# Kernel optimization log

Measured on AMD Instinct MI355X. Metric: run time of the kernel, lower is better.

The kernel has to match this reference:

```python
import jax, jax.numpy as jnp
import numpy as np

N, D, H, E = 50000, 512, 8, 3200000
DK = D // H  # 64


def setup_inputs() -> dict:
    key = jax.random.key(0)
    ks = jax.random.split(key, 12)
    x = jax.random.normal(ks[0], (N, D), dtype=jnp.float32)
    row_index = jnp.sort(jax.random.randint(ks[1], (E,), 0, N))
    col_index = jax.random.randint(ks[2], (E,), 0, N)
    att_bias = jax.random.normal(ks[3], (H, E), dtype=jnp.float32)
    # xavier-uniform-ish linear params (bias zero per module init)
    lim = np.sqrt(6.0 / (D + D)).astype(np.float32)
    def w(k):
        return jax.random.uniform(k, (D, D), minval=-lim, maxval=lim, dtype=jnp.float32)
    return {
        "x": x, "row_index": row_index, "col_index": col_index, "att_bias": att_bias,
        "Wq": w(ks[4]), "bq": jnp.zeros((D,), jnp.float32),
        "Wk": w(ks[5]), "bk": jnp.zeros((D,), jnp.float32),
        "Wv": w(ks[6]), "bv": jnp.zeros((D,), jnp.float32),
        "Wo": w(ks[7]), "bo": jnp.zeros((D,), jnp.float32),
    }


def _proj(x, W, b):
    # nn.Linear then reshape(N, H, DK).permute(1,0,2) -> [H, N, DK]
    return (x @ W.T + b).reshape(x.shape[0], H, DK).transpose(1, 0, 2)


def reference(x, row_index, col_index, att_bias, Wq, bq, Wk, bk, Wv, bv, Wo, bo):
    q = _proj(x, Wq, bq) / jnp.sqrt(jnp.float32(DK))  # [H,N,DK]
    k = _proj(x, Wk, bk)
    v = _proj(x, Wv, bv)
    n = x.shape[0]
    # masked QK^T at sparse (row,col) entries + additive sparse bias -> [H,E]
    logits = jnp.einsum("hed,hed->he", q[:, row_index], k[:, col_index]) + att_bias
    # per-row (segment) softmax over CSR rows, vmapped over heads
    seg_max = jax.vmap(lambda l: jax.ops.segment_max(l, row_index, num_segments=n))(logits)  # [H,N]
    p = jnp.exp(logits - seg_max[:, row_index])
    denom = jax.vmap(lambda pe: jax.ops.segment_sum(pe, row_index, num_segments=n))(p)  # [H,N]
    att = p / denom[:, row_index]  # [H,E]
    # sparse att @ V : scatter-add weighted value rows
    y = jax.vmap(lambda a, vc: jax.ops.segment_sum(a[:, None] * vc, row_index, num_segments=n))(
        att, v[:, col_index]
    )  # [H,N,DK]
    y = y.transpose(1, 0, 2).reshape(n, H * DK)  # [N,D]
    return y @ Wo.T + bo
```

## Files before the change

kernel.cpp:

```cpp
#include <hip/hip_runtime.h>
#include <hip/hip_bf16.h>
#include <cstddef>
#include <cstdint>


typedef __attribute__((ext_vector_type(8))) short bf16x8;
typedef __attribute__((ext_vector_type(4))) float f32x4;

#define KQ_SCALE 25.4f
#define KQ_DEQ   0.03937007874f

__device__ __forceinline__ void gload_lds16(const void* g, const void* l) {
    __builtin_amdgcn_global_load_lds(
        (const __attribute__((address_space(1))) unsigned int*)g,
        (__attribute__((address_space(3))) unsigned int*)l, 16, 0, 0);
}

__device__ __forceinline__ float bflo(unsigned u) { return __uint_as_float(u << 16); }
__device__ __forceinline__ float bfhi(unsigned u) { return __uint_as_float(u & 0xffff0000u); }
__device__ __forceinline__ float ub(unsigned u, int i) {
    return (float)((u >> (i * 8)) & 0xffu);
}

__device__ __forceinline__ void storeT(float* p, size_t i, float v) { p[i] = v; }
__device__ __forceinline__ void storeT(__hip_bfloat16* p, size_t i, float v) {
    p[i] = __float2bfloat16(v);
}
__device__ __forceinline__ void storeT(unsigned char* p, size_t i, float v) {
    const float q = fmaf(v, KQ_SCALE, 128.0f);
    p[i] = (unsigned char)__float2uint_rn(fminf(fmaxf(q, 0.f), 255.f));
}

__global__ __launch_bounds__(256) void conv_f32_bf16(
    const float* __restrict__ s, __hip_bfloat16* __restrict__ d, int n) {
    const int i = (blockIdx.x * 256 + threadIdx.x) * 8;
    if (i >= n) return;
    const float4 a = *(const float4*)(s + i);
    const float4 b = *(const float4*)(s + i + 4);
    alignas(16) __hip_bfloat16 o[8] = {
        __float2bfloat16(a.x), __float2bfloat16(a.y),
        __float2bfloat16(a.z), __float2bfloat16(a.w),
        __float2bfloat16(b.x), __float2bfloat16(b.y),
        __float2bfloat16(b.z), __float2bfloat16(b.w)};
    *(uint4*)(d + i) = *(const uint4*)o;
}

__global__ void row_start_kernel(const int* __restrict__ row_index,
                                 int* __restrict__ row_start, int n_rows, int E) {
    const int n = blockIdx.x * blockDim.x + threadIdx.x;
    if (n > n_rows) return;
    int lo = 0, hi = E;
    while (lo < hi) {
        const int mid = (lo + hi) >> 1;
        if (row_index[mid] < n) lo = mid + 1; else hi = mid;
    }
    row_start[n] = lo;
}

template <typename TO>
__global__ __launch_bounds__(256) void gemm_mfma_kernel(
    const short* __restrict__ A, const short* __restrict__ Bw,
    const float* __restrict__ bias, TO* __restrict__ C, int M, float scale) {
    __shared__ short As[128 * 32];
    __shared__ short Bs[128 * 32];
    const int t = threadIdx.x;
    const int w = t >> 6, l = t & 63;
    const int m0 = blockIdx.x * 128, n0 = blockIdx.y * 128;
    const int wrow = (w >> 1) * 64, wcol = (w & 1) * 64;
    const int fr = l & 15, fq = l >> 4;

    const int r0 = (w * 64 + l) >> 2, ko0 = ((w * 64 + l) & 3) * 8;
    int gmA0 = m0 + r0;      if (gmA0 >= M) gmA0 = M - 1;
    int gmA1 = m0 + r0 + 64; if (gmA1 >= M) gmA1 = M - 1;
    const int gnB0 = n0 + r0, gnB1 = n0 + r0 + 64;

    f32x4 acc[4][4];
#pragma unroll
    for (int mi = 0; mi < 4; ++mi)
#pragma unroll
        for (int ni = 0; ni < 4; ++ni) acc[mi][ni] = (f32x4){0.f, 0.f, 0.f, 0.f};

    for (int k0 = 0; k0 < 512; k0 += 32) {
        __syncthreads();
        gload_lds16(A + (size_t)gmA0 * 512 + k0 + ko0, As + w * 512);
        gload_lds16(A + (size_t)gmA1 * 512 + k0 + ko0, As + 2048 + w * 512);
        gload_lds16(Bw + (size_t)gnB0 * 512 + k0 + ko0, Bs + w * 512);
        gload_lds16(Bw + (size_t)gnB1 * 512 + k0 + ko0, Bs + 2048 + w * 512);
        __syncthreads();

        bf16x8 af[4], bfr[4];
#pragma unroll
        for (int mi = 0; mi < 4; ++mi)
            af[mi] = *(const bf16x8*)(As + (wrow + mi * 16 + fr) * 32 + fq * 8);
#pragma unroll
        for (int ni = 0; ni < 4; ++ni)
            bfr[ni] = *(const bf16x8*)(Bs + (wcol + ni * 16 + fr) * 32 + fq * 8);
#pragma unroll
        for (int mi = 0; mi < 4; ++mi)
#pragma unroll
            for (int ni = 0; ni < 4; ++ni)
                acc[mi][ni] = __builtin_amdgcn_mfma_f32_16x16x32_bf16(
                    af[mi], bfr[ni], acc[mi][ni], 0, 0, 0);
    }

#pragma unroll
    for (int mi = 0; mi < 4; ++mi)
#pragma unroll
        for (int ni = 0; ni < 4; ++ni)
#pragma unroll
            for (int r = 0; r < 4; ++r) {
                const int gr = m0 + wrow + mi * 16 + fq * 4 + r;
                if (gr < M) {
                    const int gc = n0 + wcol + ni * 16 + fr;
                    storeT(C, (size_t)gr * 512 + gc, (acc[mi][ni][r] + bias[gc]) * scale);
                }
            }
}

__global__ __launch_bounds__(256) void sparse_attn_kernel(
    const __hip_bfloat16* __restrict__ qb, const unsigned char* __restrict__ kq,
    const unsigned char* __restrict__ vq, const int* __restrict__ col_index,
    const float* __restrict__ att_bias, const int* __restrict__ row_start,
    __hip_bfloat16* __restrict__ yout, int E) {
    const int n = blockIdx.x;
    const int w = threadIdx.x >> 6;
    const int lane = threadIdx.x & 63;
    const int g = lane & 7;
    const int j = lane >> 3;
    const int hA = 2 * w + (g >> 2);
    const int dim0 = (g & 3) * 16;
    const int e0 = row_start[n], e1 = row_start[n + 1];

    const short* qp = (const short*)qb + (size_t)n * 512 + hA * 64 + dim0;
    float qf[16];
    {
        const uint4 a = *(const uint4*)qp;
        const uint4 b = *(const uint4*)(qp + 8);
        const unsigned* ua = (const unsigned*)&a;
        const unsigned* ubp = (const unsigned*)&b;
#pragma unroll
        for (int i = 0; i < 4; ++i) {
            qf[2 * i]     = bflo(ua[i]);
            qf[2 * i + 1] = bfhi(ua[i]);
            qf[8 + 2 * i]     = bflo(ubp[i]);
            qf[8 + 2 * i + 1] = bfhi(ubp[i]);
        }
    }
    float sumq = 0.f;
#pragma unroll
    for (int i = 0; i < 16; ++i) sumq += qf[i];
    sumq += __shfl_xor(sumq, 1, 64);
    sumq += __shfl_xor(sumq, 2, 64);
    const float qc = -128.0f * KQ_DEQ * sumq;

    const float* biasH = att_bias + (size_t)hA * (size_t)E;
    const unsigned pairoff = (unsigned)(w * 128 + g * 16);

    float acc[16];
#pragma unroll
    for (int i = 0; i < 16; ++i) acc[i] = 0.f;
    float s_lane = 0.f;

    if (e0 < e1) {
        const int e1m1 = e1 - 1;
#pragma unroll 2
        for (int base = e0; base < e1; base += 8) {
            const int e = base + j;
            const int ec = min(e, e1m1);
            const int c = col_index[ec];
            const unsigned co = ((unsigned)c << 9) + pairoff;
            const uint4 ku = *(const uint4*)(kq + co);
            const uint4 vu = *(const uint4*)(vq + co);
            const float bv = biasH[ec];

            float d = 0.f;
            {
                const unsigned* u = (const unsigned*)&ku;
#pragma unroll
                for (int i = 0; i < 4; ++i)
#pragma unroll
                    for (int b = 0; b < 4; ++b)
                        d = fmaf(qf[4 * i + b], ub(u[i], b), d);
            }
            d += __shfl_xor(d, 1, 64);
            d += __shfl_xor(d, 2, 64);
            const float lg = fmaf(KQ_DEQ, d, qc) + bv;
            const float p = (e < e1) ? __expf(lg) : 0.f;
            s_lane += p;

            {
                const unsigned* u = (const unsigned*)&vu;
#pragma unroll
                for (int i = 0; i < 4; ++i)
#pragma unroll
                    for (int b = 0; b < 4; ++b)
                        acc[4 * i + b] = fmaf(p, ub(u[i], b), acc[4 * i + b]);
            }
        }
    }

#pragma unroll
    for (int st = 8; st < 64; st <<= 1) s_lane += __shfl_xor(s_lane, st, 64);
#pragma unroll
    for (int i = 0; i < 16; ++i) {
#pragma unroll
        for (int st = 8; st < 64; st <<= 1) acc[i] += __shfl_xor(acc[i], st, 64);
    }

    float y0 = acc[0], y1 = acc[1];
#pragma unroll
    for (int t = 1; t < 8; ++t) {
        y0 = (j == t) ? acc[2 * t] : y0;
        y1 = (j == t) ? acc[2 * t + 1] : y1;
    }
    const size_t orow = (size_t)n * 512 + hA * 64 + dim0 + 2 * j;
    if (s_lane > 0.f) {
        const float inv = 1.0f / s_lane;
        yout[orow]     = __float2bfloat16(fmaf(KQ_DEQ, y0 * inv, -128.0f * KQ_DEQ));
        yout[orow + 1] = __float2bfloat16(fmaf(KQ_DEQ, y1 * inv, -128.0f * KQ_DEQ));
    } else {
        yout[orow]     = __float2bfloat16(0.f);
        yout[orow + 1] = __float2bfloat16(0.f);
    }
}

extern "C" void kernel_launch(void* const* d_in, const int* in_sizes, int n_in,
                              void* d_out, int out_size, void* d_ws, size_t ws_size,
                              hipStream_t stream) {
    const float* x         = (const float*)d_in[0];
    const int*   row_index = (const int*)d_in[1];
    const int*   col_index = (const int*)d_in[2];
    const float* att_bias  = (const float*)d_in[3];
    const float* Wq = (const float*)d_in[4];
    const float* bq = (const float*)d_in[5];
    const float* Wk = (const float*)d_in[6];
    const float* bk = (const float*)d_in[7];
    const float* Wv = (const float*)d_in[8];
    const float* bv = (const float*)d_in[9];
    const float* Wo = (const float*)d_in[10];
    const float* bo = (const float*)d_in[11];
    float* out = (float*)d_out;

    const int N = in_sizes[0] / 512;
    const int E = in_sizes[1];
    const int WN = 512 * 512;

    char* ws = (char*)d_ws;
    const size_t nb = (size_t)N * 512 * sizeof(__hip_bfloat16);
    const size_t qb8 = (size_t)N * 512;
    const size_t wb = (size_t)WN * sizeof(__hip_bfloat16);
    __hip_bfloat16* xb  = (__hip_bfloat16*)(ws);
    __hip_bfloat16* qb  = (__hip_bfloat16*)(ws + nb);
    unsigned char*  kqv = (unsigned char*)(ws + 2 * nb);
    unsigned char*  vqv = (unsigned char*)(ws + 2 * nb + qb8);
    __hip_bfloat16* wqb = (__hip_bfloat16*)(ws + 2 * nb + 2 * qb8);
    __hip_bfloat16* wkb = (__hip_bfloat16*)(ws + 2 * nb + 2 * qb8 + wb);
    __hip_bfloat16* wvb = (__hip_bfloat16*)(ws + 2 * nb + 2 * qb8 + 2 * wb);
    __hip_bfloat16* wob = (__hip_bfloat16*)(ws + 2 * nb + 2 * qb8 + 3 * wb);
    int* row_start = (int*)(ws + 2 * nb + 2 * qb8 + 4 * wb);

    conv_f32_bf16<<<(N * 512 / 8 + 255) / 256, 256, 0, stream>>>(x, xb, N * 512);
    conv_f32_bf16<<<(WN / 8 + 255) / 256, 256, 0, stream>>>(Wq, wqb, WN);
    conv_f32_bf16<<<(WN / 8 + 255) / 256, 256, 0, stream>>>(Wk, wkb, WN);
    conv_f32_bf16<<<(WN / 8 + 255) / 256, 256, 0, stream>>>(Wv, wvb, WN);
    conv_f32_bf16<<<(WN / 8 + 255) / 256, 256, 0, stream>>>(Wo, wob, WN);

    row_start_kernel<<<(N + 1 + 255) / 256, 256, 0, stream>>>(row_index, row_start, N, E);

    const dim3 gg((N + 127) / 128, 4), gb(256);
    gemm_mfma_kernel<__hip_bfloat16><<<gg, gb, 0, stream>>>(
        (const short*)xb, (const short*)wqb, bq, qb, N, 0.125f);
    gemm_mfma_kernel<unsigned char><<<gg, gb, 0, stream>>>(
        (const short*)xb, (const short*)wkb, bk, kqv, N, 1.0f);
    gemm_mfma_kernel<unsigned char><<<gg, gb, 0, stream>>>(
        (const short*)xb, (const short*)wvb, bv, vqv, N, 1.0f);

    sparse_attn_kernel<<<N, 256, 0, stream>>>(
        qb, kqv, vqv, col_index, att_bias, row_start, xb , E);

    gemm_mfma_kernel<float><<<gg, gb, 0, stream>>>(
        (const short*)xb, (const short*)wob, bo, out, N, 1.0f);
}
```

Measured before the change: 778.9 us.

## Double-buffer GEMM LDS tiles and software-pipeline sparse attention gathers

The GEMM kernel now uses two LDS buffers, issuing the global-to-LDS loads for the next K tile before computing on the current one, with one barrier per iteration instead of two. The sparse attention loop prefetches the next edge's column index, K/V bytes and bias into registers while it computes the current edge, and the bias is read with nontemporal loads. Both changes aim to hide global memory latency behind compute. The cost is double the GEMM LDS footprint and higher register pressure in the attention kernel, which may reduce occupancy. Workspace pointer names are also renamed.

New measurement: 834.3 us. 7.1% more time.

```diff
diff --git a/kernel.cpp b/kernel.cpp
--- a/kernel.cpp
+++ b/kernel.cpp
@@ -61,8 +61,8 @@
 __global__ __launch_bounds__(256) void gemm_mfma_kernel(
     const short* __restrict__ A, const short* __restrict__ Bw,
     const float* __restrict__ bias, TO* __restrict__ C, int M, float scale) {
-    __shared__ short As[128 * 32];
-    __shared__ short Bs[128 * 32];
+    __shared__ short As[2][128 * 32];
+    __shared__ short Bs[2][128 * 32];
     const int t = threadIdx.x;
     const int w = t >> 6, l = t & 63;
     const int m0 = blockIdx.x * 128, n0 = blockIdx.y * 128;
@@ -80,28 +80,38 @@
 #pragma unroll
         for (int ni = 0; ni < 4; ++ni) acc[mi][ni] = (f32x4){0.f, 0.f, 0.f, 0.f};
 
-    for (int k0 = 0; k0 < 512; k0 += 32) {
-        __syncthreads();
-        gload_lds16(A + (size_t)gmA0 * 512 + k0 + ko0, As + w * 512);
-        gload_lds16(A + (size_t)gmA1 * 512 + k0 + ko0, As + 2048 + w * 512);
-        gload_lds16(Bw + (size_t)gnB0 * 512 + k0 + ko0, Bs + w * 512);
-        gload_lds16(Bw + (size_t)gnB1 * 512 + k0 + ko0, Bs + 2048 + w * 512);
-        __syncthreads();
+#define STAGE(buf, k0)                                                        \
+    do {                                                                      \
+        gload_lds16(A + (size_t)gmA0 * 512 + (k0) + ko0, &As[buf][w * 512]);  \
+        gload_lds16(A + (size_t)gmA1 * 512 + (k0) + ko0, &As[buf][2048 + w * 512]); \
+        gload_lds16(Bw + (size_t)gnB0 * 512 + (k0) + ko0, &Bs[buf][w * 512]); \
+        gload_lds16(Bw + (size_t)gnB1 * 512 + (k0) + ko0, &Bs[buf][2048 + w * 512]); \
+    } while (0)
+
+    STAGE(0, 0);
+    __syncthreads();
+
+    for (int kt = 0; kt < 16; ++kt) {
+        const int cur = kt & 1;
+        if (kt + 1 < 16) STAGE(cur ^ 1, (kt + 1) * 32);
 
         bf16x8 af[4], bfr[4];
 #pragma unroll
         for (int mi = 0; mi < 4; ++mi)
-            af[mi] = *(const bf16x8*)(As + (wrow + mi * 16 + fr) * 32 + fq * 8);
+            af[mi] = *(const bf16x8*)(&As[cur][(wrow + mi * 16 + fr) * 32 + fq * 8]);
 #pragma unroll
         for (int ni = 0; ni < 4; ++ni)
-            bfr[ni] = *(const bf16x8*)(Bs + (wcol + ni * 16 + fr) * 32 + fq * 8);
+            bfr[ni] = *(const bf16x8*)(&Bs[cur][(wcol + ni * 16 + fr) * 32 + fq * 8]);
 #pragma unroll
         for (int mi = 0; mi < 4; ++mi)
 #pragma unroll
             for (int ni = 0; ni < 4; ++ni)
                 acc[mi][ni] = __builtin_amdgcn_mfma_f32_16x16x32_bf16(
                     af[mi], bfr[ni], acc[mi][ni], 0, 0, 0);
-    }
+
+        __syncthreads();
+    }
+#undef STAGE
 
 #pragma unroll
     for (int mi = 0; mi < 4; ++mi)
@@ -163,15 +173,24 @@
 
     if (e0 < e1) {
         const int e1m1 = e1 - 1;
-#pragma unroll 2
+        int ec = min(e0 + j, e1m1);
+        unsigned co = ((unsigned)col_index[ec] << 9) + pairoff;
+        uint4 ku = *(const uint4*)(kq + co);
+        uint4 vu = *(const uint4*)(vq + co);
+        float bv = __builtin_nontemporal_load(biasH + ec);
+        bool vld = (e0 + j) < e1;
+
         for (int base = e0; base < e1; base += 8) {
-            const int e = base + j;
-            const int ec = min(e, e1m1);
-            const int c = col_index[ec];
-            const unsigned co = ((unsigned)c << 9) + pairoff;
-            const uint4 ku = *(const uint4*)(kq + co);
-            const uint4 vu = *(const uint4*)(vq + co);
-            const float bv = biasH[ec];
+            uint4 ku_n, vu_n; float bv_n = 0.f; bool vld_n = false;
+            const int nbase = base + 8;
+            if (nbase < e1) {
+                const int ecn = min(nbase + j, e1m1);
+                const unsigned con = ((unsigned)col_index[ecn] << 9) + pairoff;
+                ku_n = *(const uint4*)(kq + con);
+                vu_n = *(const uint4*)(vq + con);
+                bv_n = __builtin_nontemporal_load(biasH + ecn);
+                vld_n = (nbase + j) < e1;
+            }
 
             float d = 0.f;
             {
@@ -185,9 +204,8 @@
             d += __shfl_xor(d, 1, 64);
             d += __shfl_xor(d, 2, 64);
             const float lg = fmaf(KQ_DEQ, d, qc) + bv;
-            const float p = (e < e1) ? __expf(lg) : 0.f;
+            const float p = vld ? __expf(lg) : 0.f;
             s_lane += p;
-
             {
                 const unsigned* u = (const unsigned*)&vu;
 #pragma unroll
@@ -196,6 +214,8 @@
                     for (int b = 0; b < 4; ++b)
                         acc[4 * i + b] = fmaf(p, ub(u[i], b), acc[4 * i + b]);
             }
+
+            ku = ku_n; vu = vu_n; bv = bv_n; vld = vld_n;
         }
     }
 
@@ -247,17 +267,17 @@
 
     char* ws = (char*)d_ws;
     const size_t nb = (size_t)N * 512 * sizeof(__hip_bfloat16);
-    const size_t qb8 = (size_t)N * 512;
+    const size_t b8 = (size_t)N * 512;
     const size_t wb = (size_t)WN * sizeof(__hip_bfloat16);
     __hip_bfloat16* xb  = (__hip_bfloat16*)(ws);
     __hip_bfloat16* qb  = (__hip_bfloat16*)(ws + nb);
-    unsigned char*  kqv = (unsigned char*)(ws + 2 * nb);
-    unsigned char*  vqv = (unsigned char*)(ws + 2 * nb + qb8);
-    __hip_bfloat16* wqb = (__hip_bfloat16*)(ws + 2 * nb + 2 * qb8);
-    __hip_bfloat16* wkb = (__hip_bfloat16*)(ws + 2 * nb + 2 * qb8 + wb);
-    __hip_bfloat16* wvb = (__hip_bfloat16*)(ws + 2 * nb + 2 * qb8 + 2 * wb);
-    __hip_bfloat16* wob = (__hip_bfloat16*)(ws + 2 * nb + 2 * qb8 + 3 * wb);
-    int* row_start = (int*)(ws + 2 * nb + 2 * qb8 + 4 * wb);
+    unsigned char*  kq8 = (unsigned char*)(ws + 2 * nb);
+    unsigned char*  vq8 = (unsigned char*)(ws + 2 * nb + b8);
+    __hip_bfloat16* wqb = (__hip_bfloat16*)(ws + 2 * nb + 2 * b8);
+    __hip_bfloat16* wkb = (__hip_bfloat16*)(ws + 2 * nb + 2 * b8 + wb);
+    __hip_bfloat16* wvb = (__hip_bfloat16*)(ws + 2 * nb + 2 * b8 + 2 * wb);
+    __hip_bfloat16* wob = (__hip_bfloat16*)(ws + 2 * nb + 2 * b8 + 3 * wb);
+    int* row_start = (int*)(ws + 2 * nb + 2 * b8 + 4 * wb);
 
     conv_f32_bf16<<<(N * 512 / 8 + 255) / 256, 256, 0, stream>>>(x, xb, N * 512);
     conv_f32_bf16<<<(WN / 8 + 255) / 256, 256, 0, stream>>>(Wq, wqb, WN);
@@ -271,12 +291,12 @@
     gemm_mfma_kernel<__hip_bfloat16><<<gg, gb, 0, stream>>>(
         (const short*)xb, (const short*)wqb, bq, qb, N, 0.125f);
     gemm_mfma_kernel<unsigned char><<<gg, gb, 0, stream>>>(
-        (const short*)xb, (const short*)wkb, bk, kqv, N, 1.0f);
+        (const short*)xb, (const short*)wkb, bk, kq8, N, 1.0f);
     gemm_mfma_kernel<unsigned char><<<gg, gb, 0, stream>>>(
-        (const short*)xb, (const short*)wvb, bv, vqv, N, 1.0f);
+        (const short*)xb, (const short*)wvb, bv, vq8, N, 1.0f);
 
     sparse_attn_kernel<<<N, 256, 0, stream>>>(
-        qb, kqv, vqv, col_index, att_bias, row_start, xb , E);
+        qb, kq8, vq8, col_index, att_bias, row_start, xb , E);
 
     gemm_mfma_kernel<float><<<gg, gb, 0, stream>>>(
         (const short*)xb, (const short*)wob, bo, out, N, 1.0f);
```

## Quantize Q to int8 per head and use sdot4 for QK dot products

Applied to the files above, without the earlier changes.

Adds a per-(node,head) int8 quantization of Q and stores K as signed int8, so the sparse attention kernel computes QK logits with integer dot4 instructions instead of unpacking bytes into float FMAs. The attention loop is also unrolled manually to process two edge groups per iteration, interleaving their loads and accumulation. This cuts ALU work and register pressure in the logit stage but adds an extra quantization kernel pass over Q and further loss of precision in the logits.

Result: slower. 831.4 us (+6.7%).

```diff
diff --git a/kernel.cpp b/kernel.cpp
--- a/kernel.cpp
+++ b/kernel.cpp
@@ -10,6 +10,20 @@
 #define KQ_SCALE 25.4f
 #define KQ_DEQ   0.03937007874f
 
+#if __has_builtin(__builtin_amdgcn_sdot4)
+__device__ __forceinline__ int SDOT4(int a, int b, int c) {
+    return __builtin_amdgcn_sdot4(a, b, c, false);
+}
+#else
+__device__ __forceinline__ int SDOT4(int a, int b, int c) {
+#pragma unroll
+    for (int i = 0; i < 4; ++i)
+        c += (int)(signed char)((unsigned)a >> (8 * i)) *
+             (int)(signed char)((unsigned)b >> (8 * i));
+    return c;
+}
+#endif
+
 __device__ __forceinline__ void gload_lds16(const void* g, const void* l) {
     __builtin_amdgcn_global_load_lds(
         (const __attribute__((address_space(1))) unsigned int*)g,
@@ -29,6 +43,9 @@
 __device__ __forceinline__ void storeT(unsigned char* p, size_t i, float v) {
     const float q = fmaf(v, KQ_SCALE, 128.0f);
     p[i] = (unsigned char)__float2uint_rn(fminf(fmaxf(q, 0.f), 255.f));
+}
+__device__ __forceinline__ void storeT(signed char* p, size_t i, float v) {
+    p[i] = (signed char)__float2int_rn(fminf(fmaxf(v, -127.f), 127.f));
 }
 
 __global__ __launch_bounds__(256) void conv_f32_bf16(
@@ -57,6 +74,22 @@
     row_start[n] = lo;
 }
 
+__global__ __launch_bounds__(256) void quant_q_kernel(
+    const __hip_bfloat16* __restrict__ qb, signed char* __restrict__ qi8,
+    float* __restrict__ qdeq, int NH) {
+    const int wid = blockIdx.x * 4 + (threadIdx.x >> 6);
+    if (wid >= NH) return;
+    const int lane = threadIdx.x & 63;
+    const size_t off = (size_t)wid * 64 + lane;
+    const float v = __bfloat162float(qb[off]);
+    float a = fabsf(v);
+#pragma unroll
+    for (int st = 1; st < 64; st <<= 1) a = fmaxf(a, __shfl_xor(a, st, 64));
+    const float scale = (a > 0.f) ? 127.0f / a : 0.f;
+    qi8[off] = (signed char)__float2int_rn(v * scale);
+    if (lane == 0) qdeq[wid] = a * (1.0f / 127.0f);
+}
+
 template <typename TO>
 __global__ __launch_bounds__(256) void gemm_mfma_kernel(
     const short* __restrict__ A, const short* __restrict__ Bw,
@@ -118,10 +151,10 @@
 }
 
 __global__ __launch_bounds__(256) void sparse_attn_kernel(
-    const __hip_bfloat16* __restrict__ qb, const unsigned char* __restrict__ kq,
-    const unsigned char* __restrict__ vq, const int* __restrict__ col_index,
-    const float* __restrict__ att_bias, const int* __restrict__ row_start,
-    __hip_bfloat16* __restrict__ yout, int E) {
+    const signed char* __restrict__ qi8, const float* __restrict__ qdeq,
+    const signed char* __restrict__ kq, const unsigned char* __restrict__ vq,
+    const int* __restrict__ col_index, const float* __restrict__ att_bias,
+    const int* __restrict__ row_start, __hip_bfloat16* __restrict__ yout, int E) {
     const int n = blockIdx.x;
     const int w = threadIdx.x >> 6;
     const int lane = threadIdx.x & 63;
@@ -131,27 +164,8 @@
     const int dim0 = (g & 3) * 16;
     const int e0 = row_start[n], e1 = row_start[n + 1];
 
-    const short* qp = (const short*)qb + (size_t)n * 512 + hA * 64 + dim0;
-    float qf[16];
-    {
-        const uint4 a = *(const uint4*)qp;
-        const uint4 b = *(const uint4*)(qp + 8);
-        const unsigned* ua = (const unsigned*)&a;
-        const unsigned* ubp = (const unsigned*)&b;
-#pragma unroll
-        for (int i = 0; i < 4; ++i) {
-            qf[2 * i]     = bflo(ua[i]);
-            qf[2 * i + 1] = bfhi(ua[i]);
-            qf[8 + 2 * i]     = bflo(ubp[i]);
-            qf[8 + 2 * i + 1] = bfhi(ubp[i]);
-        }
-    }
-    float sumq = 0.f;
-#pragma unroll
-    for (int i = 0; i < 16; ++i) sumq += qf[i];
-    sumq += __shfl_xor(sumq, 1, 64);
-    sumq += __shfl_xor(sumq, 2, 64);
-    const float qc = -128.0f * KQ_DEQ * sumq;
+    const int4 qu = *(const int4*)(qi8 + (size_t)n * 512 + hA * 64 + dim0);
+    const float dsc = qdeq[(size_t)n * 8 + hA] * KQ_DEQ;
 
     const float* biasH = att_bias + (size_t)hA * (size_t)E;
     const unsigned pairoff = (unsigned)(w * 128 + g * 16);
@@ -163,38 +177,49 @@
 
     if (e0 < e1) {
         const int e1m1 = e1 - 1;
-#pragma unroll 2
-        for (int base = e0; base < e1; base += 8) {
-            const int e = base + j;
-            const int ec = min(e, e1m1);
-            const int c = col_index[ec];
-            const unsigned co = ((unsigned)c << 9) + pairoff;
-            const uint4 ku = *(const uint4*)(kq + co);
-            const uint4 vu = *(const uint4*)(vq + co);
-            const float bv = biasH[ec];
-
-            float d = 0.f;
+        for (int base = e0; base < e1; base += 16) {
+            const int eA = base + j, eB = base + 8 + j;
+            const int ecA = min(eA, e1m1), ecB = min(eB, e1m1);
+            const int cA = col_index[ecA], cB = col_index[ecB];
+            const unsigned coA = ((unsigned)cA << 9) + pairoff;
+            const unsigned coB = ((unsigned)cB << 9) + pairoff;
+            const int4 kuA = *(const int4*)(kq + coA);
+            const uint4 vuA = *(const uint4*)(vq + coA);
+            const int4 kuB = *(const int4*)(kq + coB);
+            const uint4 vuB = *(const uint4*)(vq + coB);
+            const float bvA = biasH[ecA];
+            const float bvB = biasH[ecB];
+
+            int a0 = 0, a1 = 0, b0 = 0, b1 = 0;
+            a0 = SDOT4(qu.x, kuA.x, a0);
+            a1 = SDOT4(qu.y, kuA.y, a1);
+            b0 = SDOT4(qu.x, kuB.x, b0);
+            b1 = SDOT4(qu.y, kuB.y, b1);
+            a0 = SDOT4(qu.z, kuA.z, a0);
+            a1 = SDOT4(qu.w, kuA.w, a1);
+            b0 = SDOT4(qu.z, kuB.z, b0);
+            b1 = SDOT4(qu.w, kuB.w, b1);
+            int idA = a0 + a1, idB = b0 + b1;
+            idA += __shfl_xor(idA, 1, 64);
+            idB += __shfl_xor(idB, 1, 64);
+            idA += __shfl_xor(idA, 2, 64);
+            idB += __shfl_xor(idB, 2, 64);
+            const float lgA = fmaf((float)idA, dsc, bvA);
+            const float lgB = fmaf((float)idB, dsc, bvB);
+            const float pA = (eA < e1) ? __expf(lgA) : 0.f;
+            const float pB = (eB < e1) ? __expf(lgB) : 0.f;
+            s_lane += pA + pB;
+
             {
-                const unsigned* u = (const unsigned*)&ku;
+                const unsigned* uA = (const unsigned*)&vuA;
+                const unsigned* uB = (const unsigned*)&vuB;
 #pragma unroll
                 for (int i = 0; i < 4; ++i)
 #pragma unroll
-                    for (int b = 0; b < 4; ++b)
-                        d = fmaf(qf[4 * i + b], ub(u[i], b), d);
-            }
-            d += __shfl_xor(d, 1, 64);
-            d += __shfl_xor(d, 2, 64);
-            const float lg = fmaf(KQ_DEQ, d, qc) + bv;
-            const float p = (e < e1) ? __expf(lg) : 0.f;
-            s_lane += p;
-
-            {
-                const unsigned* u = (const unsigned*)&vu;
-#pragma unroll
-                for (int i = 0; i < 4; ++i)
-#pragma unroll
-                    for (int b = 0; b < 4; ++b)
-                        acc[4 * i + b] = fmaf(p, ub(u[i], b), acc[4 * i + b]);
+                    for (int b = 0; b < 4; ++b) {
+                        acc[4 * i + b] = fmaf(pA, ub(uA[i], b), acc[4 * i + b]);
+                        acc[4 * i + b] = fmaf(pB, ub(uB[i], b), acc[4 * i + b]);
+                    }
             }
         }
     }
@@ -247,17 +272,19 @@
 
     char* ws = (char*)d_ws;
     const size_t nb = (size_t)N * 512 * sizeof(__hip_bfloat16);
-    const size_t qb8 = (size_t)N * 512;
+    const size_t b8 = (size_t)N * 512;
     const size_t wb = (size_t)WN * sizeof(__hip_bfloat16);
     __hip_bfloat16* xb  = (__hip_bfloat16*)(ws);
     __hip_bfloat16* qb  = (__hip_bfloat16*)(ws + nb);
-    unsigned char*  kqv = (unsigned char*)(ws + 2 * nb);
-    unsigned char*  vqv = (unsigned char*)(ws + 2 * nb + qb8);
-    __hip_bfloat16* wqb = (__hip_bfloat16*)(ws + 2 * nb + 2 * qb8);
-    __hip_bfloat16* wkb = (__hip_bfloat16*)(ws + 2 * nb + 2 * qb8 + wb);
-    __hip_bfloat16* wvb = (__hip_bfloat16*)(ws + 2 * nb + 2 * qb8 + 2 * wb);
-    __hip_bfloat16* wob = (__hip_bfloat16*)(ws + 2 * nb + 2 * qb8 + 3 * wb);
-    int* row_start = (int*)(ws + 2 * nb + 2 * qb8 + 4 * wb);
+    signed char*    kq8 = (signed char*)(ws + 2 * nb);
+    unsigned char*  vq8 = (unsigned char*)(ws + 2 * nb + b8);
+    signed char*    qi8 = (signed char*)(ws + 2 * nb + 2 * b8);
+    __hip_bfloat16* wqb = (__hip_bfloat16*)(ws + 2 * nb + 3 * b8);
+    __hip_bfloat16* wkb = (__hip_bfloat16*)(ws + 2 * nb + 3 * b8 + wb);
+    __hip_bfloat16* wvb = (__hip_bfloat16*)(ws + 2 * nb + 3 * b8 + 2 * wb);
+    __hip_bfloat16* wob = (__hip_bfloat16*)(ws + 2 * nb + 3 * b8 + 3 * wb);
+    float* qdeq = (float*)(ws + 2 * nb + 3 * b8 + 4 * wb);
+    int* row_start = (int*)(ws + 2 * nb + 3 * b8 + 4 * wb + (size_t)N * 8 * 4);
 
     conv_f32_bf16<<<(N * 512 / 8 + 255) / 256, 256, 0, stream>>>(x, xb, N * 512);
     conv_f32_bf16<<<(WN / 8 + 255) / 256, 256, 0, stream>>>(Wq, wqb, WN);
@@ -270,13 +297,15 @@
     const dim3 gg((N + 127) / 128, 4), gb(256);
     gemm_mfma_kernel<__hip_bfloat16><<<gg, gb, 0, stream>>>(
         (const short*)xb, (const short*)wqb, bq, qb, N, 0.125f);
+    gemm_mfma_kernel<signed char><<<gg, gb, 0, stream>>>(
+        (const short*)xb, (const short*)wkb, bk, kq8, N, KQ_SCALE);
     gemm_mfma_kernel<unsigned char><<<gg, gb, 0, stream>>>(
-        (const short*)xb, (const short*)wkb, bk, kqv, N, 1.0f);
-    gemm_mfma_kernel<unsigned char><<<gg, gb, 0, stream>>>(
-        (const short*)xb, (const short*)wvb, bv, vqv, N, 1.0f);
+        (const short*)xb, (const short*)wvb, bv, vq8, N, 1.0f);
+
+    quant_q_kernel<<<(N * 8 + 3) / 4, 256, 0, stream>>>(qb, qi8, qdeq, N * 8);
 
     sparse_attn_kernel<<<N, 256, 0, stream>>>(
-        qb, kqv, vqv, col_index, att_bias, row_start, xb , E);
+        qi8, qdeq, kq8, vq8, col_index, att_bias, row_start, xb , E);
 
     gemm_mfma_kernel<float><<<gg, gb, 0, stream>>>(
         (const short*)xb, (const short*)wob, bo, out, N, 1.0f);
```
